# Optimization experiments

Hardware: AMD Instinct MI355X
Metric: run time of the kernel (lower is better)

Reference implementation:

```python
import jax, jax.numpy as jnp
import numpy as np

WS = 7      # window size
NH = 4      # n_heads
EPS = 1e-5  # torch LayerNorm default


def setup_inputs() -> dict:
    key = jax.random.key(0)
    ks = jax.random.split(key, 4)
    B, H, W, C = 16, 112, 112, 128
    N = H * W
    s = 0.02
    return {
        "x": jax.random.normal(ks[0], (B, N, C), jnp.float32),
        "ln_gamma": jnp.ones((C,), jnp.float32),
        "ln_beta": jnp.zeros((C,), jnp.float32),
        "w_qkv": jax.random.normal(ks[1], (3 * C, C), jnp.float32) * s,
        "b_qkv": jnp.zeros((3 * C,), jnp.float32),
        "w_mo": jax.random.normal(ks[2], (C, C), jnp.float32) * s,
        "b_mo": jnp.zeros((C,), jnp.float32),
        "w_out": jax.random.normal(ks[3], (C, C), jnp.float32) * s,
        "b_out": jnp.zeros((C,), jnp.float32),
        "H": 112,
        "W": 112,
    }


def reference(x, ln_gamma, ln_beta, w_qkv, b_qkv, w_mo, b_mo, w_out, b_out, H, W):
    B, N, C = x.shape
    hd = C // NH
    # pre-norm LayerNorm
    mu = jnp.mean(x, axis=-1, keepdims=True)
    var = jnp.mean((x - mu) ** 2, axis=-1, keepdims=True)
    normed = (x - mu) * jax.lax.rsqrt(var + EPS) * ln_gamma + ln_beta
    normed = normed.reshape(B, H, W, C)
    # pad to multiple of window size (static H, W)
    pad_h = (-H) % WS
    pad_w = (-W) % WS
    if pad_h or pad_w:
        normed = jnp.pad(normed, ((0, 0), (0, pad_h), (0, pad_w), (0, 0)))
    Hp, Wp = H + pad_h, W + pad_w
    # window partition -> [B*nWh*nWw, ws*ws, C]
    win = normed.reshape(B, Hp // WS, WS, Wp // WS, WS, C)
    win = win.transpose(0, 1, 3, 2, 4, 5).reshape(-1, WS * WS, C)
    # MHA (self-attention), torch Linear convention: y = x @ W.T + b
    qkv = win @ w_qkv.T + b_qkv
    q, k, v = jnp.split(qkv, 3, axis=-1)
    def heads(t):  # [nW, T, C] -> [nW, NH, T, hd]
        return t.reshape(t.shape[0], WS * WS, NH, hd).transpose(0, 2, 1, 3)
    q, k, v = heads(q), heads(k), heads(v)
    scores = jnp.einsum("whqd,whkd->whqk", q, k) / jnp.sqrt(jnp.float32(hd))
    attn = jax.nn.softmax(scores, axis=-1)
    o = jnp.einsum("whqk,whkd->whqd", attn, v)
    o = o.transpose(0, 2, 1, 3).reshape(-1, WS * WS, C)
    o = o @ w_mo.T + b_mo
    # window merge -> [B, Hp, Wp, C], crop padding
    o = o.reshape(B, Hp // WS, Wp // WS, WS, WS, C)
    o = o.transpose(0, 1, 3, 2, 4, 5).reshape(B, Hp, Wp, C)
    o = o[:, :H, :W, :].reshape(B, N, C)
    # final projection + residual
    return x + o @ w_out.T + b_out
```

## Files before the change

kernel.cpp:

```cpp
#include <hip/hip_runtime.h>
#include <hip/hip_bf16.h>

namespace {

typedef __attribute__((ext_vector_type(8))) short bf16x8;
typedef __attribute__((ext_vector_type(4))) float f32x4;

union BF8U { unsigned u[4]; bf16x8 v; };

__device__ __forceinline__ unsigned pk2(float a, float b) {
    union { __hip_bfloat162 h2; unsigned u; } c;
    c.h2 = __float22bfloat162_rn(float2{a, b});
    return c.u;
}
__device__ __forceinline__ unsigned short b1(float f) {
    union { __hip_bfloat16 h; unsigned short s; } c;
    c.h = __float2bfloat16(f);
    return c.s;
}
__device__ __forceinline__ int SWZ(int byteoff, int row) {
    return byteoff ^ ((row & 7) << 4);
}

constexpr int SX  = 0;
constexpr int SAO = 16384;
constexpr int LDS_BYTES = 32768;


template<bool USEWS>
__device__ __forceinline__ bf16x8 load_wfrag(const unsigned short* wsb, const float* wf, int idx) {
    if constexpr (USEWS) {
        return *(const bf16x8*)(wsb + idx);
    } else {
        const float4 f0 = *(const float4*)(wf + idx);
        const float4 f1 = *(const float4*)(wf + idx + 4);
        bf16x8 r;
        r[0] = (short)b1(f0.x); r[1] = (short)b1(f0.y);
        r[2] = (short)b1(f0.z); r[3] = (short)b1(f0.w);
        r[4] = (short)b1(f1.x); r[5] = (short)b1(f1.y);
        r[6] = (short)b1(f1.z); r[7] = (short)b1(f1.w);
        return r;
    }
}

__global__ void conv_w2(const float* __restrict__ wqkv, const float* __restrict__ bqkv,
                        const float* __restrict__ wmo,  const float* __restrict__ bmo,
                        const float* __restrict__ wout, const float* __restrict__ bout,
                        const float* __restrict__ lng,  const float* __restrict__ lnb,
                        unsigned short* __restrict__ dst) {
    float* fb = (float*)(dst + 65536);
    const int bid = blockIdx.x, t = threadIdx.x;
    if (bid < 192) {
        const int idx = bid * 256 + t;
        dst[idx] = b1(wqkv[idx] * lng[idx & 127]);
    } else if (bid < 256) {
        const int e = (bid - 192) * 256 + t;
        const int o = e >> 7, i = e & 127;
        const float* wo = wout + o * 128;
        float s = 0.f;
        for (int k = 0; k < 128; ++k) s += wo[k] * wmo[k * 128 + i];
        dst[49152 + e] = b1(s);
    } else if (bid < 258) {
        const int o = (bid - 256) * 256 + t;
        if (o < 384) {
            const float* wr = wqkv + o * 128;
            float s = 0.f;
            for (int i = 0; i < 128; ++i) s += wr[i] * lnb[i];
            fb[o] = bqkv[o] + s;
        }
    } else {
        if (t < 128) {
            const float* wo = wout + t * 128;
            float s = 0.f;
            for (int k = 0; k < 128; ++k) s += wo[k] * bmo[k];
            fb[384 + t] = bout[t] + s;
        }
    }
}

template<bool USEWS>
__global__ __launch_bounds__(256, 3)
void swin_mfma(const float* __restrict__ x,
               const float* __restrict__ lng, const float* __restrict__ lnb,
               const float* __restrict__ wqkv, const float* __restrict__ bqkv,
               const float* __restrict__ wmo,  const float* __restrict__ bmo,
               const float* __restrict__ wout, const float* __restrict__ bout,
               const unsigned short* __restrict__ wsb,
               float* __restrict__ out)
{
    __shared__ char lds[LDS_BYTES];

    const float* fb = USEWS ? (const float*)(wsb + 65536) : nullptr;

    const int wid  = blockIdx.x;
    const int b    = wid >> 8;
    const int wh   = (wid >> 4) & 15;
    const int ww   = wid & 15;
    const int t    = threadIdx.x;
    const int lane = t & 63;
    const int h    = t >> 6;
    const int lr   = lane & 15;
    const int g    = lane >> 4;
    const int hb   = h * 32;

    const size_t base = ((size_t)(b * 112 + wh * 7) * 112 + ww * 7) * 128;

    if (t < 240) *(f32x4*)(lds + SX + 49 * 256 + t * 16) = f32x4{0.f, 0.f, 0.f, 0.f};
    {
        const int tok = t >> 2, q4 = t & 3;
        if (tok < 49) {
            const float* xr = x + base + (size_t)((tok / 7) * 112 + (tok % 7)) * 128;
            float4 xv[8];
            float s1 = 0.f, s2 = 0.f;
            #pragma unroll
            for (int j = 0; j < 8; ++j) {
                xv[j] = *(const float4*)(xr + j * 16 + q4 * 4);
                s1 += xv[j].x + xv[j].y + xv[j].z + xv[j].w;
                s2 += xv[j].x * xv[j].x + xv[j].y * xv[j].y
                    + xv[j].z * xv[j].z + xv[j].w * xv[j].w;
            }
            s1 += __shfl_xor(s1, 1); s1 += __shfl_xor(s1, 2);
            s2 += __shfl_xor(s2, 1); s2 += __shfl_xor(s2, 2);
            const float mu  = s1 * (1.f / 128.f);
            const float inv = rsqrtf(s2 * (1.f / 128.f) - mu * mu + 1e-5f);
            #pragma unroll
            for (int j = 0; j < 8; ++j) {
                float y0, y1, y2, y3;
                if constexpr (USEWS) {
                    y0 = (xv[j].x - mu) * inv;
                    y1 = (xv[j].y - mu) * inv;
                    y2 = (xv[j].z - mu) * inv;
                    y3 = (xv[j].w - mu) * inv;
                } else {
                    const float4 gm = *(const float4*)(lng + j * 16 + q4 * 4);
                    const float4 bt = *(const float4*)(lnb + j * 16 + q4 * 4);
                    y0 = (xv[j].x - mu) * inv * gm.x + bt.x;
                    y1 = (xv[j].y - mu) * inv * gm.y + bt.y;
                    y2 = (xv[j].z - mu) * inv * gm.z + bt.z;
                    y3 = (xv[j].w - mu) * inv * gm.w + bt.w;
                }
                uint2 w; w.x = pk2(y0, y1); w.y = pk2(y2, y3);
                *(uint2*)(lds + SX + tok * 256 + SWZ(j * 32 + q4 * 8, tok)) = w;
            }
        }
    }
    __syncthreads();

    unsigned pkQ[4][2][2], pkK[4][2][2];
    {
        f32x4 aQ[2][4], aK[2][4];
        #pragma unroll
        for (int ot = 0; ot < 2; ++ot)
            #pragma unroll
            for (int tt = 0; tt < 4; ++tt) {
                aQ[ot][tt] = f32x4{0.f, 0.f, 0.f, 0.f};
                aK[ot][tt] = f32x4{0.f, 0.f, 0.f, 0.f};
            }
        #pragma unroll
        for (int kk = 0; kk < 4; ++kk) {
            bf16x8 xa[4];
            #pragma unroll
            for (int tt = 0; tt < 4; ++tt) {
                int row = tt * 16 + lr;
                xa[tt] = *(bf16x8*)(lds + SX + row * 256 + SWZ(kk * 64 + g * 16, row));
            }
            #pragma unroll
            for (int ot = 0; ot < 2; ++ot) {
                bf16x8 wq = load_wfrag<USEWS>(wsb, wqkv, (hb + ot * 16 + lr) * 128 + kk * 32 + g * 8);
                bf16x8 wk = load_wfrag<USEWS>(wsb, wqkv, (128 + hb + ot * 16 + lr) * 128 + kk * 32 + g * 8);
                #pragma unroll
                for (int tt = 0; tt < 4; ++tt) {
                    aQ[ot][tt] = __builtin_amdgcn_mfma_f32_16x16x32_bf16(wq, xa[tt], aQ[ot][tt], 0, 0, 0);
                    aK[ot][tt] = __builtin_amdgcn_mfma_f32_16x16x32_bf16(wk, xa[tt], aK[ot][tt], 0, 0, 0);
                }
            }
        }
        #pragma unroll
        for (int ot = 0; ot < 2; ++ot) {
            float4 bq, bk;
            if constexpr (USEWS) {
                bq = *(const float4*)(fb + hb + ot * 16 + g * 4);
                bk = *(const float4*)(fb + 128 + hb + ot * 16 + g * 4);
            } else {
                bq = *(const float4*)(bqkv + hb + ot * 16 + g * 4);
                bk = *(const float4*)(bqkv + 128 + hb + ot * 16 + g * 4);
            }
            #pragma unroll
            for (int nti = 0; nti < 4; ++nti) {
                const float q0 = (aQ[ot][nti][0] + bq.x) * 0.17677669529663687f;
                const float q1 = (aQ[ot][nti][1] + bq.y) * 0.17677669529663687f;
                const float q2 = (aQ[ot][nti][2] + bq.z) * 0.17677669529663687f;
                const float q3 = (aQ[ot][nti][3] + bq.w) * 0.17677669529663687f;
                pkQ[nti][ot][0] = pk2(q0, q1); pkQ[nti][ot][1] = pk2(q2, q3);
                pkK[nti][ot][0] = pk2(aK[ot][nti][0] + bk.x, aK[ot][nti][1] + bk.y);
                pkK[nti][ot][1] = pk2(aK[ot][nti][2] + bk.z, aK[ot][nti][3] + bk.w);
            }
        }
    }

    unsigned pkV[2][4][2];
    {
        f32x4 aV[4][2];
        #pragma unroll
        for (int mt = 0; mt < 4; ++mt) {
            aV[mt][0] = f32x4{0.f, 0.f, 0.f, 0.f};
            aV[mt][1] = f32x4{0.f, 0.f, 0.f, 0.f};
        }
        #pragma unroll
        for (int kk = 0; kk < 4; ++kk) {
            bf16x8 xa[4];
            #pragma unroll
            for (int tt = 0; tt < 4; ++tt) {
                int row = tt * 16 + lr;
                xa[tt] = *(bf16x8*)(lds + SX + row * 256 + SWZ(kk * 64 + g * 16, row));
            }
            bf16x8 wv0 = load_wfrag<USEWS>(wsb, wqkv, (256 + hb + lr) * 128 + kk * 32 + g * 8);
            bf16x8 wv1 = load_wfrag<USEWS>(wsb, wqkv, (256 + hb + 16 + lr) * 128 + kk * 32 + g * 8);
            #pragma unroll
            for (int mt = 0; mt < 4; ++mt) {
                aV[mt][0] = __builtin_amdgcn_mfma_f32_16x16x32_bf16(xa[mt], wv0, aV[mt][0], 0, 0, 0);
                aV[mt][1] = __builtin_amdgcn_mfma_f32_16x16x32_bf16(xa[mt], wv1, aV[mt][1], 0, 0, 0);
            }
        }
        const float bv0 = USEWS ? fb[256 + hb + lr]      : bqkv[256 + hb + lr];
        const float bv1 = USEWS ? fb[256 + hb + 16 + lr] : bqkv[256 + hb + 16 + lr];
        #pragma unroll
        for (int mt = 0; mt < 4; ++mt) {
            pkV[0][mt][0] = pk2(aV[mt][0][0] + bv0, aV[mt][0][1] + bv0);
            pkV[0][mt][1] = pk2(aV[mt][0][2] + bv0, aV[mt][0][3] + bv0);
            pkV[1][mt][0] = pk2(aV[mt][1][0] + bv1, aV[mt][1][1] + bv1);
            pkV[1][mt][1] = pk2(aV[mt][1][2] + bv1, aV[mt][1][3] + bv1);
        }
    }

    const int s01  = lr + ((lane & 16) ? 32 : 0);
    const int s23  = s01 + 16;
    const bool hiT = (lane & 32) != 0;
    auto RD4 = [&](unsigned e0, unsigned e1, unsigned o0, unsigned o1) -> bf16x8 {
        BF8U r;
        const unsigned v0 = hiT ? o0 : e0;
        const unsigned v1 = hiT ? o1 : e1;
        r.u[0] = (unsigned)__shfl((int)v0, s01);
        r.u[1] = (unsigned)__shfl((int)v1, s01);
        r.u[2] = (unsigned)__shfl((int)v0, s23);
        r.u[3] = (unsigned)__shfl((int)v1, s23);
        return r.v;
    };

    unsigned pkP[4][4][2];
    {
        f32x4 S[4][4];
        bf16x8 qb[4];
        #pragma unroll
        for (int nti = 0; nti < 4; ++nti)
            qb[nti] = RD4(pkQ[nti][0][0], pkQ[nti][0][1], pkQ[nti][1][0], pkQ[nti][1][1]);
        #pragma unroll
        for (int mtj = 0; mtj < 4; ++mtj) {
            bf16x8 ka = RD4(pkK[mtj][0][0], pkK[mtj][0][1], pkK[mtj][1][0], pkK[mtj][1][1]);
            #pragma unroll
            for (int nti = 0; nti < 4; ++nti)
                S[mtj][nti] = __builtin_amdgcn_mfma_f32_16x16x32_bf16(ka, qb[nti],
                                                                      f32x4{0.f, 0.f, 0.f, 0.f}, 0, 0, 0);
        }
        #pragma unroll
        for (int nti = 0; nti < 4; ++nti)
            #pragma unroll
            for (int r = 0; r < 4; ++r)
                if (r != 0 || g != 0) S[3][nti][r] = -1e30f;

        #pragma unroll
        for (int nti = 0; nti < 4; ++nti) {
            float m = S[0][nti][0];
            #pragma unroll
            for (int mtj = 0; mtj < 4; ++mtj)
                #pragma unroll
                for (int r = 0; r < 4; ++r) m = fmaxf(m, S[mtj][nti][r]);
            m = fmaxf(m, __shfl_xor(m, 16));
            m = fmaxf(m, __shfl_xor(m, 32));
            float sum = 0.f;
            #pragma unroll
            for (int mtj = 0; mtj < 4; ++mtj)
                #pragma unroll
                for (int r = 0; r < 4; ++r) {
                    const float p = __expf(S[mtj][nti][r] - m);
                    S[mtj][nti][r] = p;
                    sum += p;
                }
            sum += __shfl_xor(sum, 16);
            sum += __shfl_xor(sum, 32);
            const float rinv = 1.0f / sum;
            #pragma unroll
            for (int mtj = 0; mtj < 4; ++mtj) {
                pkP[nti][mtj][0] = pk2(S[mtj][nti][0] * rinv, S[mtj][nti][1] * rinv);
                pkP[nti][mtj][1] = pk2(S[mtj][nti][2] * rinv, S[mtj][nti][3] * rinv);
            }
        }
    }

    {
        bf16x8 vb[2][2];
        #pragma unroll
        for (int kk = 0; kk < 2; ++kk)
            #pragma unroll
            for (int ntd = 0; ntd < 2; ++ntd)
                vb[kk][ntd] = RD4(pkV[ntd][2 * kk][0], pkV[ntd][2 * kk][1],
                                  pkV[ntd][2 * kk + 1][0], pkV[ntd][2 * kk + 1][1]);
        #pragma unroll
        for (int mti = 0; mti < 4; ++mti) {
            bf16x8 pa0 = RD4(pkP[mti][0][0], pkP[mti][0][1], pkP[mti][1][0], pkP[mti][1][1]);
            bf16x8 pa1 = RD4(pkP[mti][2][0], pkP[mti][2][1], pkP[mti][3][0], pkP[mti][3][1]);
            f32x4 O0 = f32x4{0.f, 0.f, 0.f, 0.f}, O1 = O0;
            O0 = __builtin_amdgcn_mfma_f32_16x16x32_bf16(pa0, vb[0][0], O0, 0, 0, 0);
            O0 = __builtin_amdgcn_mfma_f32_16x16x32_bf16(pa1, vb[1][0], O0, 0, 0, 0);
            O1 = __builtin_amdgcn_mfma_f32_16x16x32_bf16(pa0, vb[0][1], O1, 0, 0, 0);
            O1 = __builtin_amdgcn_mfma_f32_16x16x32_bf16(pa1, vb[1][1], O1, 0, 0, 0);
            #pragma unroll
            for (int r = 0; r < 4; ++r) {
                const int i = mti * 16 + g * 4 + r;
                *(unsigned short*)(lds + SAO + i * 256 + SWZ((hb + lr) * 2, i))      = b1(O0[r]);
                *(unsigned short*)(lds + SAO + i * 256 + SWZ((hb + 16 + lr) * 2, i)) = b1(O1[r]);
            }
        }
    }
    __syncthreads();

    if constexpr (USEWS) {
        bf16x8 a[4][4];
        #pragma unroll
        for (int mt = 0; mt < 4; ++mt)
            #pragma unroll
            for (int kk = 0; kk < 4; ++kk) {
                int row = mt * 16 + lr;
                a[mt][kk] = *(bf16x8*)(lds + SAO + row * 256 + SWZ(g * 16 + kk * 64, row));
            }
        #pragma unroll
        for (int ntl = 0; ntl < 2; ++ntl) {
            const int oc = hb + ntl * 16 + lr;
            bf16x8 bfr[4];
            #pragma unroll
            for (int kk = 0; kk < 4; ++kk)
                bfr[kk] = *(const bf16x8*)(wsb + 49152 + oc * 128 + kk * 32 + g * 8);
            f32x4 acc[4];
            #pragma unroll
            for (int mt = 0; mt < 4; ++mt) acc[mt] = f32x4{0.f, 0.f, 0.f, 0.f};
            #pragma unroll
            for (int kk = 0; kk < 4; ++kk)
                #pragma unroll
                for (int mt = 0; mt < 4; ++mt)
                    acc[mt] = __builtin_amdgcn_mfma_f32_16x16x32_bf16(a[mt][kk], bfr[kk], acc[mt], 0, 0, 0);
            const float bias = fb[384 + oc];
            #pragma unroll
            for (int mt = 0; mt < 4; ++mt)
                #pragma unroll
                for (int r = 0; r < 4; ++r) {
                    const int row = mt * 16 + g * 4 + r;
                    if (row < 49) {
                        const size_t gi = base + (size_t)((row / 7) * 112 + (row % 7)) * 128 + oc;
                        out[gi] = x[gi] + acc[mt][r] + bias;
                    }
                }
        }
    } else {
        {
            bf16x8 a[4][4];
            #pragma unroll
            for (int mt = 0; mt < 4; ++mt)
                #pragma unroll
                for (int kk = 0; kk < 4; ++kk) {
                    int row = mt * 16 + lr;
                    a[mt][kk] = *(bf16x8*)(lds + SAO + row * 256 + SWZ(g * 16 + kk * 64, row));
                }
            #pragma unroll
            for (int ntl = 0; ntl < 2; ++ntl) {
                const int oc = hb + ntl * 16 + lr;
                bf16x8 bfr[4];
                #pragma unroll
                for (int kk = 0; kk < 4; ++kk)
                    bfr[kk] = load_wfrag<false>(nullptr, wmo, oc * 128 + kk * 32 + g * 8);
                f32x4 acc[4];
                #pragma unroll
                for (int mt = 0; mt < 4; ++mt) acc[mt] = f32x4{0.f, 0.f, 0.f, 0.f};
                #pragma unroll
                for (int kk = 0; kk < 4; ++kk)
                    #pragma unroll
                    for (int mt = 0; mt < 4; ++mt)
                        acc[mt] = __builtin_amdgcn_mfma_f32_16x16x32_bf16(a[mt][kk], bfr[kk], acc[mt], 0, 0, 0);
                const float bias = bmo[oc];
                #pragma unroll
                for (int mt = 0; mt < 4; ++mt)
                    #pragma unroll
                    for (int r = 0; r < 4; ++r) {
                        int row = mt * 16 + g * 4 + r;
                        *(unsigned short*)(lds + SX + row * 256 + SWZ(oc * 2, row)) = b1(acc[mt][r] + bias);
                    }
            }
        }
        __syncthreads();
        {
            bf16x8 a[4][4];
            #pragma unroll
            for (int mt = 0; mt < 4; ++mt)
                #pragma unroll
                for (int kk = 0; kk < 4; ++kk) {
                    int row = mt * 16 + lr;
                    a[mt][kk] = *(bf16x8*)(lds + SX + row * 256 + SWZ(g * 16 + kk * 64, row));
                }
            #pragma unroll
            for (int ntl = 0; ntl < 2; ++ntl) {
                const int oc = hb + ntl * 16 + lr;
                bf16x8 bfr[4];
                #pragma unroll
                for (int kk = 0; kk < 4; ++kk)
                    bfr[kk] = load_wfrag<false>(nullptr, wout, oc * 128 + kk * 32 + g * 8);
                f32x4 acc[4];
                #pragma unroll
                for (int mt = 0; mt < 4; ++mt) acc[mt] = f32x4{0.f, 0.f, 0.f, 0.f};
                #pragma unroll
                for (int kk = 0; kk < 4; ++kk)
                    #pragma unroll
                    for (int mt = 0; mt < 4; ++mt)
                        acc[mt] = __builtin_amdgcn_mfma_f32_16x16x32_bf16(a[mt][kk], bfr[kk], acc[mt], 0, 0, 0);
                const float bias = bout[oc];
                #pragma unroll
                for (int mt = 0; mt < 4; ++mt)
                    #pragma unroll
                    for (int r = 0; r < 4; ++r) {
                        const int row = mt * 16 + g * 4 + r;
                        if (row < 49) {
                            const size_t gi = base + (size_t)((row / 7) * 112 + (row % 7)) * 128 + oc;
                            out[gi] = x[gi] + acc[mt][r] + bias;
                        }
                    }
            }
        }
    }
}

}

extern "C" void kernel_launch(void* const* d_in, const int* in_sizes, int n_in,
                              void* d_out, int out_size, void* d_ws, size_t ws_size,
                              hipStream_t stream) {
    const float* x    = (const float*)d_in[0];
    const float* lng  = (const float*)d_in[1];
    const float* lnb  = (const float*)d_in[2];
    const float* wqkv = (const float*)d_in[3];
    const float* bqkv = (const float*)d_in[4];
    const float* wmo  = (const float*)d_in[5];
    const float* bmo  = (const float*)d_in[6];
    const float* wout = (const float*)d_in[7];
    const float* bout = (const float*)d_in[8];
    float* out = (float*)d_out;

    if (ws_size >= 133120) {
        unsigned short* wsb = (unsigned short*)d_ws;
        conv_w2<<<259, 256, 0, stream>>>(wqkv, bqkv, wmo, bmo, wout, bout, lng, lnb, wsb);
        swin_mfma<true><<<4096, 256, 0, stream>>>(x, lng, lnb, wqkv, bqkv, wmo, bmo,
                                                  wout, bout, wsb, out);
    } else {
        swin_mfma<false><<<4096, 256, 0, stream>>>(x, lng, lnb, wqkv, bqkv, wmo, bmo,
                                                   wout, bout, nullptr, out);
    }
}
```

Before: 115.9 us.

## Restructure attention stages to cut register pressure and raise occupancy

Splits the fused Q/K projection into separate Q and K passes, defers the V projection until after softmax, processes the score matrix in two halves, and restructures the final projection to stream A fragments per k-step. Compiler barriers keep these stages apart so fewer accumulators are live at once. Launch bounds go from 3 to 4 blocks per CU to use the freed registers. The cost is re-reading the LDS X tile for each projection pass, plus a risk of spills if the register cap is too tight.

```diff
diff --git a/kernel.cpp b/kernel.cpp
--- a/kernel.cpp
+++ b/kernel.cpp
@@ -79,7 +79,7 @@
 }
 
 template<bool USEWS>
-__global__ __launch_bounds__(256, 3)
+__global__ __launch_bounds__(256, 4)
 void swin_mfma(const float* __restrict__ x,
                const float* __restrict__ lng, const float* __restrict__ lnb,
                const float* __restrict__ wqkv, const float* __restrict__ bqkv,
@@ -146,93 +146,6 @@
     }
     __syncthreads();
 
-    unsigned pkQ[4][2][2], pkK[4][2][2];
-    {
-        f32x4 aQ[2][4], aK[2][4];
-        #pragma unroll
-        for (int ot = 0; ot < 2; ++ot)
-            #pragma unroll
-            for (int tt = 0; tt < 4; ++tt) {
-                aQ[ot][tt] = f32x4{0.f, 0.f, 0.f, 0.f};
-                aK[ot][tt] = f32x4{0.f, 0.f, 0.f, 0.f};
-            }
-        #pragma unroll
-        for (int kk = 0; kk < 4; ++kk) {
-            bf16x8 xa[4];
-            #pragma unroll
-            for (int tt = 0; tt < 4; ++tt) {
-                int row = tt * 16 + lr;
-                xa[tt] = *(bf16x8*)(lds + SX + row * 256 + SWZ(kk * 64 + g * 16, row));
-            }
-            #pragma unroll
-            for (int ot = 0; ot < 2; ++ot) {
-                bf16x8 wq = load_wfrag<USEWS>(wsb, wqkv, (hb + ot * 16 + lr) * 128 + kk * 32 + g * 8);
-                bf16x8 wk = load_wfrag<USEWS>(wsb, wqkv, (128 + hb + ot * 16 + lr) * 128 + kk * 32 + g * 8);
-                #pragma unroll
-                for (int tt = 0; tt < 4; ++tt) {
-                    aQ[ot][tt] = __builtin_amdgcn_mfma_f32_16x16x32_bf16(wq, xa[tt], aQ[ot][tt], 0, 0, 0);
-                    aK[ot][tt] = __builtin_amdgcn_mfma_f32_16x16x32_bf16(wk, xa[tt], aK[ot][tt], 0, 0, 0);
-                }
-            }
-        }
-        #pragma unroll
-        for (int ot = 0; ot < 2; ++ot) {
-            float4 bq, bk;
-            if constexpr (USEWS) {
-                bq = *(const float4*)(fb + hb + ot * 16 + g * 4);
-                bk = *(const float4*)(fb + 128 + hb + ot * 16 + g * 4);
-            } else {
-                bq = *(const float4*)(bqkv + hb + ot * 16 + g * 4);
-                bk = *(const float4*)(bqkv + 128 + hb + ot * 16 + g * 4);
-            }
-            #pragma unroll
-            for (int nti = 0; nti < 4; ++nti) {
-                const float q0 = (aQ[ot][nti][0] + bq.x) * 0.17677669529663687f;
-                const float q1 = (aQ[ot][nti][1] + bq.y) * 0.17677669529663687f;
-                const float q2 = (aQ[ot][nti][2] + bq.z) * 0.17677669529663687f;
-                const float q3 = (aQ[ot][nti][3] + bq.w) * 0.17677669529663687f;
-                pkQ[nti][ot][0] = pk2(q0, q1); pkQ[nti][ot][1] = pk2(q2, q3);
-                pkK[nti][ot][0] = pk2(aK[ot][nti][0] + bk.x, aK[ot][nti][1] + bk.y);
-                pkK[nti][ot][1] = pk2(aK[ot][nti][2] + bk.z, aK[ot][nti][3] + bk.w);
-            }
-        }
-    }
-
-    unsigned pkV[2][4][2];
-    {
-        f32x4 aV[4][2];
-        #pragma unroll
-        for (int mt = 0; mt < 4; ++mt) {
-            aV[mt][0] = f32x4{0.f, 0.f, 0.f, 0.f};
-            aV[mt][1] = f32x4{0.f, 0.f, 0.f, 0.f};
-        }
-        #pragma unroll
-        for (int kk = 0; kk < 4; ++kk) {
-            bf16x8 xa[4];
-            #pragma unroll
-            for (int tt = 0; tt < 4; ++tt) {
-                int row = tt * 16 + lr;
-                xa[tt] = *(bf16x8*)(lds + SX + row * 256 + SWZ(kk * 64 + g * 16, row));
-            }
-            bf16x8 wv0 = load_wfrag<USEWS>(wsb, wqkv, (256 + hb + lr) * 128 + kk * 32 + g * 8);
-            bf16x8 wv1 = load_wfrag<USEWS>(wsb, wqkv, (256 + hb + 16 + lr) * 128 + kk * 32 + g * 8);
-            #pragma unroll
-            for (int mt = 0; mt < 4; ++mt) {
-                aV[mt][0] = __builtin_amdgcn_mfma_f32_16x16x32_bf16(xa[mt], wv0, aV[mt][0], 0, 0, 0);
-                aV[mt][1] = __builtin_amdgcn_mfma_f32_16x16x32_bf16(xa[mt], wv1, aV[mt][1], 0, 0, 0);
-            }
-        }
-        const float bv0 = USEWS ? fb[256 + hb + lr]      : bqkv[256 + hb + lr];
-        const float bv1 = USEWS ? fb[256 + hb + 16 + lr] : bqkv[256 + hb + 16 + lr];
-        #pragma unroll
-        for (int mt = 0; mt < 4; ++mt) {
-            pkV[0][mt][0] = pk2(aV[mt][0][0] + bv0, aV[mt][0][1] + bv0);
-            pkV[0][mt][1] = pk2(aV[mt][0][2] + bv0, aV[mt][0][3] + bv0);
-            pkV[1][mt][0] = pk2(aV[mt][1][0] + bv1, aV[mt][1][1] + bv1);
-            pkV[1][mt][1] = pk2(aV[mt][1][2] + bv1, aV[mt][1][3] + bv1);
-        }
-    }
-
     const int s01  = lr + ((lane & 16) ? 32 : 0);
     const int s23  = s01 + 16;
     const bool hiT = (lane & 32) != 0;
@@ -247,34 +160,115 @@
         return r.v;
     };
 
+    unsigned pkQ[4][2][2];
+    {
+        f32x4 aQ[2][4];
+        #pragma unroll
+        for (int ot = 0; ot < 2; ++ot)
+            #pragma unroll
+            for (int tt = 0; tt < 4; ++tt) aQ[ot][tt] = f32x4{0.f, 0.f, 0.f, 0.f};
+        #pragma unroll
+        for (int kk = 0; kk < 4; ++kk) {
+            bf16x8 xa[4];
+            #pragma unroll
+            for (int tt = 0; tt < 4; ++tt) {
+                int row = tt * 16 + lr;
+                xa[tt] = *(bf16x8*)(lds + SX + row * 256 + SWZ(kk * 64 + g * 16, row));
+            }
+            #pragma unroll
+            for (int ot = 0; ot < 2; ++ot) {
+                bf16x8 wq = load_wfrag<USEWS>(wsb, wqkv, (hb + ot * 16 + lr) * 128 + kk * 32 + g * 8);
+                #pragma unroll
+                for (int tt = 0; tt < 4; ++tt)
+                    aQ[ot][tt] = __builtin_amdgcn_mfma_f32_16x16x32_bf16(wq, xa[tt], aQ[ot][tt], 0, 0, 0);
+            }
+        }
+        #pragma unroll
+        for (int ot = 0; ot < 2; ++ot) {
+            float4 bq;
+            if constexpr (USEWS) bq = *(const float4*)(fb + hb + ot * 16 + g * 4);
+            else                 bq = *(const float4*)(bqkv + hb + ot * 16 + g * 4);
+            #pragma unroll
+            for (int nti = 0; nti < 4; ++nti) {
+                const float q0 = (aQ[ot][nti][0] + bq.x) * 0.17677669529663687f;
+                const float q1 = (aQ[ot][nti][1] + bq.y) * 0.17677669529663687f;
+                const float q2 = (aQ[ot][nti][2] + bq.z) * 0.17677669529663687f;
+                const float q3 = (aQ[ot][nti][3] + bq.w) * 0.17677669529663687f;
+                pkQ[nti][ot][0] = pk2(q0, q1); pkQ[nti][ot][1] = pk2(q2, q3);
+            }
+        }
+    }
+    asm volatile("" ::: "memory");
+
+    unsigned pkK[4][2][2];
+    {
+        f32x4 aK[2][4];
+        #pragma unroll
+        for (int ot = 0; ot < 2; ++ot)
+            #pragma unroll
+            for (int tt = 0; tt < 4; ++tt) aK[ot][tt] = f32x4{0.f, 0.f, 0.f, 0.f};
+        #pragma unroll
+        for (int kk = 0; kk < 4; ++kk) {
+            bf16x8 xa[4];
+            #pragma unroll
+            for (int tt = 0; tt < 4; ++tt) {
+                int row = tt * 16 + lr;
+                xa[tt] = *(bf16x8*)(lds + SX + row * 256 + SWZ(kk * 64 + g * 16, row));
+            }
+            #pragma unroll
+            for (int ot = 0; ot < 2; ++ot) {
+                bf16x8 wk = load_wfrag<USEWS>(wsb, wqkv, (128 + hb + ot * 16 + lr) * 128 + kk * 32 + g * 8);
+                #pragma unroll
+                for (int tt = 0; tt < 4; ++tt)
+                    aK[ot][tt] = __builtin_amdgcn_mfma_f32_16x16x32_bf16(wk, xa[tt], aK[ot][tt], 0, 0, 0);
+            }
+        }
+        #pragma unroll
+        for (int ot = 0; ot < 2; ++ot) {
+            float4 bk;
+            if constexpr (USEWS) bk = *(const float4*)(fb + 128 + hb + ot * 16 + g * 4);
+            else                 bk = *(const float4*)(bqkv + 128 + hb + ot * 16 + g * 4);
+            #pragma unroll
+            for (int nti = 0; nti < 4; ++nti) {
+                pkK[nti][ot][0] = pk2(aK[ot][nti][0] + bk.x, aK[ot][nti][1] + bk.y);
+                pkK[nti][ot][1] = pk2(aK[ot][nti][2] + bk.z, aK[ot][nti][3] + bk.w);
+            }
+        }
+    }
+    asm volatile("" ::: "memory");
+
     unsigned pkP[4][4][2];
-    {
-        f32x4 S[4][4];
-        bf16x8 qb[4];
-        #pragma unroll
-        for (int nti = 0; nti < 4; ++nti)
-            qb[nti] = RD4(pkQ[nti][0][0], pkQ[nti][0][1], pkQ[nti][1][0], pkQ[nti][1][1]);
+    #pragma unroll
+    for (int half = 0; half < 2; ++half) {
+        f32x4 S[4][2];
+        bf16x8 qb[2];
+        #pragma unroll
+        for (int ni = 0; ni < 2; ++ni) {
+            const int nti = half * 2 + ni;
+            qb[ni] = RD4(pkQ[nti][0][0], pkQ[nti][0][1], pkQ[nti][1][0], pkQ[nti][1][1]);
+        }
         #pragma unroll
         for (int mtj = 0; mtj < 4; ++mtj) {
             bf16x8 ka = RD4(pkK[mtj][0][0], pkK[mtj][0][1], pkK[mtj][1][0], pkK[mtj][1][1]);
             #pragma unroll
-            for (int nti = 0; nti < 4; ++nti)
-                S[mtj][nti] = __builtin_amdgcn_mfma_f32_16x16x32_bf16(ka, qb[nti],
-                                                                      f32x4{0.f, 0.f, 0.f, 0.f}, 0, 0, 0);
-        }
-        #pragma unroll
-        for (int nti = 0; nti < 4; ++nti)
+            for (int ni = 0; ni < 2; ++ni)
+                S[mtj][ni] = __builtin_amdgcn_mfma_f32_16x16x32_bf16(ka, qb[ni],
+                                                                     f32x4{0.f, 0.f, 0.f, 0.f}, 0, 0, 0);
+        }
+        #pragma unroll
+        for (int ni = 0; ni < 2; ++ni)
             #pragma unroll
             for (int r = 0; r < 4; ++r)
-                if (r != 0 || g != 0) S[3][nti][r] = -1e30f;
-
-        #pragma unroll
-        for (int nti = 0; nti < 4; ++nti) {
-            float m = S[0][nti][0];
+                if (r != 0 || g != 0) S[3][ni][r] = -1e30f;
+
+        #pragma unroll
+        for (int ni = 0; ni < 2; ++ni) {
+            const int nti = half * 2 + ni;
+            float m = S[0][ni][0];
             #pragma unroll
             for (int mtj = 0; mtj < 4; ++mtj)
                 #pragma unroll
-                for (int r = 0; r < 4; ++r) m = fmaxf(m, S[mtj][nti][r]);
+                for (int r = 0; r < 4; ++r) m = fmaxf(m, S[mtj][ni][r]);
             m = fmaxf(m, __shfl_xor(m, 16));
             m = fmaxf(m, __shfl_xor(m, 32));
             float sum = 0.f;
@@ -282,8 +276,8 @@
             for (int mtj = 0; mtj < 4; ++mtj)
                 #pragma unroll
                 for (int r = 0; r < 4; ++r) {
-                    const float p = __expf(S[mtj][nti][r] - m);
-                    S[mtj][nti][r] = p;
+                    const float p = __expf(S[mtj][ni][r] - m);
+                    S[mtj][ni][r] = p;
                     sum += p;
                 }
             sum += __shfl_xor(sum, 16);
@@ -291,11 +285,48 @@
             const float rinv = 1.0f / sum;
             #pragma unroll
             for (int mtj = 0; mtj < 4; ++mtj) {
-                pkP[nti][mtj][0] = pk2(S[mtj][nti][0] * rinv, S[mtj][nti][1] * rinv);
-                pkP[nti][mtj][1] = pk2(S[mtj][nti][2] * rinv, S[mtj][nti][3] * rinv);
-            }
-        }
-    }
+                pkP[nti][mtj][0] = pk2(S[mtj][ni][0] * rinv, S[mtj][ni][1] * rinv);
+                pkP[nti][mtj][1] = pk2(S[mtj][ni][2] * rinv, S[mtj][ni][3] * rinv);
+            }
+        }
+    }
+    asm volatile("" ::: "memory");
+
+    unsigned pkV[2][4][2];
+    {
+        f32x4 aV[4][2];
+        #pragma unroll
+        for (int mt = 0; mt < 4; ++mt) {
+            aV[mt][0] = f32x4{0.f, 0.f, 0.f, 0.f};
+            aV[mt][1] = f32x4{0.f, 0.f, 0.f, 0.f};
+        }
+        #pragma unroll
+        for (int kk = 0; kk < 4; ++kk) {
+            bf16x8 xa[4];
+            #pragma unroll
+            for (int tt = 0; tt < 4; ++tt) {
+                int row = tt * 16 + lr;
+                xa[tt] = *(bf16x8*)(lds + SX + row * 256 + SWZ(kk * 64 + g * 16, row));
+            }
+            bf16x8 wv0 = load_wfrag<USEWS>(wsb, wqkv, (256 + hb + lr) * 128 + kk * 32 + g * 8);
+            bf16x8 wv1 = load_wfrag<USEWS>(wsb, wqkv, (256 + hb + 16 + lr) * 128 + kk * 32 + g * 8);
+            #pragma unroll
+            for (int mt = 0; mt < 4; ++mt) {
+                aV[mt][0] = __builtin_amdgcn_mfma_f32_16x16x32_bf16(xa[mt], wv0, aV[mt][0], 0, 0, 0);
+                aV[mt][1] = __builtin_amdgcn_mfma_f32_16x16x32_bf16(xa[mt], wv1, aV[mt][1], 0, 0, 0);
+            }
+        }
+        const float bv0 = USEWS ? fb[256 + hb + lr]      : bqkv[256 + hb + lr];
+        const float bv1 = USEWS ? fb[256 + hb + 16 + lr] : bqkv[256 + hb + 16 + lr];
+        #pragma unroll
+        for (int mt = 0; mt < 4; ++mt) {
+            pkV[0][mt][0] = pk2(aV[mt][0][0] + bv0, aV[mt][0][1] + bv0);
+            pkV[0][mt][1] = pk2(aV[mt][0][2] + bv0, aV[mt][0][3] + bv0);
+            pkV[1][mt][0] = pk2(aV[mt][1][0] + bv1, aV[mt][1][1] + bv1);
+            pkV[1][mt][1] = pk2(aV[mt][1][2] + bv1, aV[mt][1][3] + bv1);
+        }
+    }
+    asm volatile("" ::: "memory");
 
     {
         bf16x8 vb[2][2];
@@ -325,29 +356,31 @@
     __syncthreads();
 
     if constexpr (USEWS) {
-        bf16x8 a[4][4];
-        #pragma unroll
-        for (int mt = 0; mt < 4; ++mt)
-            #pragma unroll
-            for (int kk = 0; kk < 4; ++kk) {
+        f32x4 acc[4][2];
+        #pragma unroll
+        for (int mt = 0; mt < 4; ++mt) {
+            acc[mt][0] = f32x4{0.f, 0.f, 0.f, 0.f};
+            acc[mt][1] = f32x4{0.f, 0.f, 0.f, 0.f};
+        }
+        #pragma unroll
+        for (int kk = 0; kk < 4; ++kk) {
+            bf16x8 a4[4];
+            #pragma unroll
+            for (int mt = 0; mt < 4; ++mt) {
                 int row = mt * 16 + lr;
-                a[mt][kk] = *(bf16x8*)(lds + SAO + row * 256 + SWZ(g * 16 + kk * 64, row));
-            }
+                a4[mt] = *(bf16x8*)(lds + SAO + row * 256 + SWZ(g * 16 + kk * 64, row));
+            }
+            bf16x8 b0 = *(const bf16x8*)(wsb + 49152 + (hb + lr) * 128 + kk * 32 + g * 8);
+            bf16x8 b1f = *(const bf16x8*)(wsb + 49152 + (hb + 16 + lr) * 128 + kk * 32 + g * 8);
+            #pragma unroll
+            for (int mt = 0; mt < 4; ++mt) {
+                acc[mt][0] = __builtin_amdgcn_mfma_f32_16x16x32_bf16(a4[mt], b0,  acc[mt][0], 0, 0, 0);
+                acc[mt][1] = __builtin_amdgcn_mfma_f32_16x16x32_bf16(a4[mt], b1f, acc[mt][1], 0, 0, 0);
+            }
+        }
         #pragma unroll
         for (int ntl = 0; ntl < 2; ++ntl) {
             const int oc = hb + ntl * 16 + lr;
-            bf16x8 bfr[4];
-            #pragma unroll
-            for (int kk = 0; kk < 4; ++kk)
-                bfr[kk] = *(const bf16x8*)(wsb + 49152 + oc * 128 + kk * 32 + g * 8);
-            f32x4 acc[4];
-            #pragma unroll
-            for (int mt = 0; mt < 4; ++mt) acc[mt] = f32x4{0.f, 0.f, 0.f, 0.f};
-            #pragma unroll
-            for (int kk = 0; kk < 4; ++kk)
-                #pragma unroll
-                for (int mt = 0; mt < 4; ++mt)
-                    acc[mt] = __builtin_amdgcn_mfma_f32_16x16x32_bf16(a[mt][kk], bfr[kk], acc[mt], 0, 0, 0);
             const float bias = fb[384 + oc];
             #pragma unroll
             for (int mt = 0; mt < 4; ++mt)
@@ -356,7 +389,7 @@
                     const int row = mt * 16 + g * 4 + r;
                     if (row < 49) {
                         const size_t gi = base + (size_t)((row / 7) * 112 + (row % 7)) * 128 + oc;
-                        out[gi] = x[gi] + acc[mt][r] + bias;
+                        out[gi] = x[gi] + acc[mt][ntl][r] + bias;
                     }
                 }
         }
```

New measurement: 103.1 us. 1.12x faster.
